# Optimization experiments

Measured on AMD Instinct MI355X. Metric: run time of the kernel, lower is better.

## Reference

```python
import jax, jax.numpy as jnp
import numpy as np

B, IC, H, W = 1024, 3, 32, 32
E, NC = 8, 100            # num_experts, num_classes
GCH, ECH = 16, 32         # gate hidden channels, expert hidden channels
K = 3                     # conv kernel size


def _conv2d(x, w):
    # x: [B,Cin,H,W], w: [Cout,Cin,kh,kw] -> [B,Cout,H,W] (SAME padding, stride 1)
    return jax.lax.conv_general_dilated(
        x, w, window_strides=(1, 1), padding='SAME',
        dimension_numbers=('NCHW', 'OIHW', 'NCHW'))


def setup_inputs() -> dict:
    key = jax.random.key(0)
    ks = jax.random.split(key, 9)
    init = lambda k, shape, fan: (jax.random.normal(k, shape, jnp.float32)
                                  * np.float32(1.0 / np.sqrt(fan)))
    return {
        'x': jax.random.normal(ks[0], (B, IC, H, W), jnp.float32),
        # GatingNetwork: conv(3->16) + relu + global-avg-pool + linear(16->E) + softmax
        'gate_conv_w': init(ks[1], (GCH, IC, K, K), IC * K * K),
        'gate_conv_b': jnp.zeros((GCH,), jnp.float32),
        'gate_lin_w': init(ks[2], (E, GCH), GCH),
        'gate_lin_b': jnp.zeros((E,), jnp.float32),
        # ExpertLayer (per expert): conv(3->32) + relu + global-avg-pool + linear(32->NC)
        'exp_conv_w': init(ks[3], (E, ECH, IC, K, K), IC * K * K),
        'exp_conv_b': jnp.zeros((E, ECH), jnp.float32),
        'exp_lin_w': init(ks[4], (E, NC, ECH), ECH),
        'exp_lin_b': jnp.zeros((E, NC), jnp.float32),
    }


def reference(x, gate_conv_w, gate_conv_b, gate_lin_w, gate_lin_b,
              exp_conv_w, exp_conv_b, exp_lin_w, exp_lin_b):
    # ---- Router: softmax gate over experts ----
    g = jax.nn.relu(_conv2d(x, gate_conv_w) + gate_conv_b[None, :, None, None])
    g = g.mean(axis=(2, 3))                                   # [B,GCH]
    weights = jax.nn.softmax(g @ gate_lin_w.T + gate_lin_b, axis=1)  # [B,E]
    best = jnp.argmax(weights, axis=1)                        # [B] hard top-1

    # ---- All experts as one fused conv (dense compute, then hard select) ----
    e, ch, ic, kh, kw = exp_conv_w.shape
    w_all = exp_conv_w.reshape(e * ch, ic, kh, kw)
    feat = _conv2d(x, w_all)                                  # [B,E*ECH,H,W]
    feat = feat.reshape(x.shape[0], e, ch, feat.shape[2], feat.shape[3])
    feat = jax.nn.relu(feat + exp_conv_b[None, :, :, None, None])
    pooled = feat.mean(axis=(3, 4))                           # [B,E,ECH]
    out_all = jnp.einsum('bec,enc->ben', pooled, exp_lin_w) + exp_lin_b[None]  # [B,E,NC]

    # Combine: each row gets only its argmax expert's output (others -> zero grad)
    final = jnp.take_along_axis(out_all, best[:, None, None], axis=1)[:, 0, :]  # [B,NC]
    return (final, weights)
```

## Files before the change

### kernel.cpp

```cpp
#include <hip/hip_runtime.h>
#include <math.h>

#define NB 1024
#define IC 3
#define HW 32
#define GCH 16
#define ECH 32
#define NE 8
#define NC 100

#define CS 38
#define RS2 114
#define NTX 3876

typedef __attribute__((ext_vector_type(8))) short bf16x8;
typedef __attribute__((ext_vector_type(4))) int   int4v;
typedef __attribute__((ext_vector_type(4))) float f32x4;

__device__ inline short f2bf(float f) {
    unsigned u = __float_as_uint(f);
    unsigned r = (u + 0x7FFF + ((u >> 16) & 1)) >> 16;
    return (short)r;
}
__device__ inline float bf2f(short h) {
    return __uint_as_float(((unsigned)(unsigned short)h) << 16);
}

__global__ __launch_bounds__(256) void moe_fused_kernel(
    const float* __restrict__ x,
    const float* __restrict__ gcw,
    const float* __restrict__ gcb,
    const float* __restrict__ glw,
    const float* __restrict__ glb,
    const float* __restrict__ ecw,
    const float* __restrict__ ecb,
    const float* __restrict__ elw,
    const float* __restrict__ elb,
    float* __restrict__ out_final,
    float* __restrict__ out_w)
{
    __shared__ __align__(16) int xil[NTX];
    __shared__ float red2[4][32];
    __shared__ float pg[GCH];
    __shared__ float pe[ECH];
    __shared__ int s_best;

    const int t = threadIdx.x;
    const int b = blockIdx.x;
    const int lane = t & 63;
    const int wid = t >> 6;
    const int r15 = lane & 15;
    const int kg = lane >> 4;
    const bool k3 = (kg == 3);
    const int kgoff = k3 ? 0 : kg * CS;

    for (int i = t; i < NTX / 4; i += 256) ((int4*)xil)[i] = make_int4(0, 0, 0, 0);

    bf16x8 gbh, gbl;
    #pragma unroll
    for (int r = 0; r < 8; ++r) {
        float w = 0.f;
        if (kg < 3) w = gcw[r15 * 27 + kg * 9 + r];
        else if (r < 3) w = gcw[r15 * 27 + r * 9 + 8];
        short h = f2bf(w);
        gbh[r] = h;
        gbl[r] = f2bf(w - bf2f(h));
    }
    const float gb = gcb[r15];

    __syncthreads();

    const float* xb = x + (size_t)b * (IC * HW * HW);
    #pragma unroll
    for (int i3 = 0; i3 < 3; ++i3) {
        int i = t + i3 * 256;
        float4 v = ((const float4*)xb)[i];
        int ci = i >> 8, rem = i & 255, row = rem >> 3, x4 = (rem & 7) << 2;
        int T = (row + 1) * RS2 + ci * CS + x4 + 2;
        short h0 = f2bf(v.x), h1 = f2bf(v.y), h2 = f2bf(v.z), h3 = f2bf(v.w);
        int t0 = (unsigned short)h0 | ((unsigned)(unsigned short)f2bf(v.x - bf2f(h0)) << 16);
        int t1 = (unsigned short)h1 | ((unsigned)(unsigned short)f2bf(v.y - bf2f(h1)) << 16);
        int t2 = (unsigned short)h2 | ((unsigned)(unsigned short)f2bf(v.z - bf2f(h2)) << 16);
        int t3 = (unsigned short)h3 | ((unsigned)(unsigned short)f2bf(v.w - bf2f(h3)) << 16);
        *(int2*)&xil[T]     = make_int2(t0, t1);
        *(int2*)&xil[T + 2] = make_int2(t2, t3);
    }

    __syncthreads();

    float sg = 0.f;
    #pragma unroll 2
    for (int m = 0; m < 16; ++m) {
        int px = (wid << 8) + (m << 4) + r15;
        int rowbase = (px >> 5) * RS2 + (px & 31) + 1;
        int vA = rowbase + kgoff;
        int vB = rowbase + 2 * RS2;
        int T0 = xil[vA];           int T1 = xil[vA + 1];
        int T2 = xil[vA + 2];       int T3 = xil[vA + RS2];
        int T4 = xil[vA + RS2 + 1]; int T5 = xil[vA + RS2 + 2];
        int T6 = xil[vA + 2 * RS2]; int T7 = xil[vA + 2 * RS2 + 1];
        int U0 = xil[vB + 2];       int U1 = xil[vB + 2 + CS];
        int U2 = xil[vB + 2 + 2 * CS];
        int X0 = k3 ? U0 : T0;
        int X1 = k3 ? U1 : T1;
        int X2 = k3 ? U2 : T2;
        int4v ahd = { (int)__builtin_amdgcn_perm(X1, X0, 0x05040100u),
                      (int)__builtin_amdgcn_perm(T3, X2, 0x05040100u),
                      (int)__builtin_amdgcn_perm(T5, T4, 0x05040100u),
                      (int)__builtin_amdgcn_perm(T7, T6, 0x05040100u) };
        int4v ald = { (int)__builtin_amdgcn_perm(X1, X0, 0x07060302u),
                      (int)__builtin_amdgcn_perm(T3, X2, 0x07060302u),
                      (int)__builtin_amdgcn_perm(T5, T4, 0x07060302u),
                      (int)__builtin_amdgcn_perm(T7, T6, 0x07060302u) };
        bf16x8 ah = __builtin_bit_cast(bf16x8, ahd);
        bf16x8 al = __builtin_bit_cast(bf16x8, ald);
        f32x4 d = {0.f, 0.f, 0.f, 0.f};
        d = __builtin_amdgcn_mfma_f32_16x16x32_bf16(al, gbh, d, 0, 0, 0);
        d = __builtin_amdgcn_mfma_f32_16x16x32_bf16(ah, gbl, d, 0, 0, 0);
        d = __builtin_amdgcn_mfma_f32_16x16x32_bf16(ah, gbh, d, 0, 0, 0);
        sg += fmaxf(d[0] + gb, 0.f) + fmaxf(d[1] + gb, 0.f) +
              fmaxf(d[2] + gb, 0.f) + fmaxf(d[3] + gb, 0.f);
    }
    {
        float v = sg;
        v += __shfl_xor(v, 16);
        v += __shfl_xor(v, 32);
        if (lane < 16) red2[wid][lane] = v;
    }
    __syncthreads();
    if (t < GCH)
        pg[t] = (red2[0][t] + red2[1][t] + red2[2][t] + red2[3][t]) * (1.f / 1024.f);
    __syncthreads();

    if (t < NE) {
        float acc = glb[t];
        #pragma unroll
        for (int c = 0; c < GCH; ++c) acc += pg[c] * glw[t * GCH + c];
        float m = acc;
        #pragma unroll
        for (int o = 1; o < NE; o <<= 1) m = fmaxf(m, __shfl_xor(m, o));
        float ex = expf(acc - m);
        float s = ex;
        #pragma unroll
        for (int o = 1; o < NE; o <<= 1) s += __shfl_xor(s, o);
        out_w[(size_t)b * NE + t] = ex / s;
        float mv = acc; int mi = t;
        #pragma unroll
        for (int o = 1; o < NE; o <<= 1) {
            float ov = __shfl_xor(mv, o);
            int   oi = __shfl_xor(mi, o);
            if (ov > mv || (ov == mv && oi < mi)) { mv = ov; mi = oi; }
        }
        if (t == 0) s_best = mi;
    }
    __syncthreads();
    const int e = __builtin_amdgcn_readfirstlane(s_best);

    const float* ewp = ecw + (size_t)e * (ECH * 27);
    const float* ebp = ecb + (size_t)e * ECH;

    bf16x8 bfr0, bfr1;
    #pragma unroll
    for (int r = 0; r < 8; ++r) {
        float w0 = 0.f, w1 = 0.f;
        if (kg < 3) {
            w0 = ewp[r15 * 27 + kg * 9 + r];
            w1 = ewp[(16 + r15) * 27 + kg * 9 + r];
        } else if (r < 3) {
            w0 = ewp[r15 * 27 + r * 9 + 8];
            w1 = ewp[(16 + r15) * 27 + r * 9 + 8];
        }
        bfr0[r] = f2bf(w0);
        bfr1[r] = f2bf(w1);
    }
    const float b0 = ebp[r15];
    const float b1 = ebp[16 + r15];

    float s0 = 0.f, s1 = 0.f;
    #pragma unroll 2
    for (int m = 0; m < 16; ++m) {
        int px = (wid << 8) + (m << 4) + r15;
        int rowbase = (px >> 5) * RS2 + (px & 31) + 1;
        int vA = rowbase + kgoff;
        int vB = rowbase + 2 * RS2;
        int T0 = xil[vA];           int T1 = xil[vA + 1];
        int T2 = xil[vA + 2];       int T3 = xil[vA + RS2];
        int T4 = xil[vA + RS2 + 1]; int T5 = xil[vA + RS2 + 2];
        int T6 = xil[vA + 2 * RS2]; int T7 = xil[vA + 2 * RS2 + 1];
        int U0 = xil[vB + 2];       int U1 = xil[vB + 2 + CS];
        int U2 = xil[vB + 2 + 2 * CS];
        int X0 = k3 ? U0 : T0;
        int X1 = k3 ? U1 : T1;
        int X2 = k3 ? U2 : T2;
        int4v ahd = { (int)__builtin_amdgcn_perm(X1, X0, 0x05040100u),
                      (int)__builtin_amdgcn_perm(T3, X2, 0x05040100u),
                      (int)__builtin_amdgcn_perm(T5, T4, 0x05040100u),
                      (int)__builtin_amdgcn_perm(T7, T6, 0x05040100u) };
        bf16x8 a = __builtin_bit_cast(bf16x8, ahd);
        f32x4 z = {0.f, 0.f, 0.f, 0.f};
        f32x4 d0 = __builtin_amdgcn_mfma_f32_16x16x32_bf16(a, bfr0, z, 0, 0, 0);
        f32x4 d1 = __builtin_amdgcn_mfma_f32_16x16x32_bf16(a, bfr1, z, 0, 0, 0);
        s0 += fmaxf(d0[0] + b0, 0.f) + fmaxf(d0[1] + b0, 0.f) +
              fmaxf(d0[2] + b0, 0.f) + fmaxf(d0[3] + b0, 0.f);
        s1 += fmaxf(d1[0] + b1, 0.f) + fmaxf(d1[1] + b1, 0.f) +
              fmaxf(d1[2] + b1, 0.f) + fmaxf(d1[3] + b1, 0.f);
    }
    {
        float v0 = s0, v1 = s1;
        v0 += __shfl_xor(v0, 16); v0 += __shfl_xor(v0, 32);
        v1 += __shfl_xor(v1, 16); v1 += __shfl_xor(v1, 32);
        if (lane < 16) { red2[wid][lane] = v0; red2[wid][lane + 16] = v1; }
    }
    __syncthreads();
    if (t < ECH)
        pe[t] = (red2[0][t] + red2[1][t] + red2[2][t] + red2[3][t]) * (1.f / 1024.f);
    __syncthreads();

    if (t < NC) {
        const float* lw = elw + ((size_t)e * NC + t) * ECH;
        float acc = elb[e * NC + t];
        #pragma unroll
        for (int c = 0; c < ECH; ++c) acc += pe[c] * lw[c];
        out_final[(size_t)b * NC + t] = acc;
    }
}

extern "C" void kernel_launch(void* const* d_in, const int* in_sizes, int n_in,
                              void* d_out, int out_size, void* d_ws, size_t ws_size,
                              hipStream_t stream) {
    const float* x   = (const float*)d_in[0];
    const float* gcw = (const float*)d_in[1];
    const float* gcb = (const float*)d_in[2];
    const float* glw = (const float*)d_in[3];
    const float* glb = (const float*)d_in[4];
    const float* ecw = (const float*)d_in[5];
    const float* ecb = (const float*)d_in[6];
    const float* elw = (const float*)d_in[7];
    const float* elb = (const float*)d_in[8];

    float* out_final = (float*)d_out;
    float* out_w     = (float*)d_out + NB * NC;

    hipLaunchKernelGGL(moe_fused_kernel, dim3(NB), dim3(256), 0, stream,
                       x, gcw, gcb, glw, glb, ecw, ecb, elw, elb,
                       out_final, out_w);
}
```

Before: 19.83 us.

## Process two samples per block to amortize setup and interleave MFMA chains

Each 256-thread block now handles two batch samples instead of one, which halves the grid to 512 blocks and doubles the LDS tile. Gate and expert convolutions for both samples are interleaved in the same loop, so independent MFMA chains can overlap, and the weight-fragment setup and barriers are shared across two samples. The cost is more registers and LDS per block and only 512 blocks, which may leave some of the 256 CUs with fewer waves to hide latency.

New measurement: 23.37 us. 17.9% more time.

```diff
diff --git a/kernel.cpp b/kernel.cpp
--- a/kernel.cpp
+++ b/kernel.cpp
@@ -39,14 +39,15 @@
     float* __restrict__ out_final,
     float* __restrict__ out_w)
 {
-    __shared__ __align__(16) int xil[NTX];
-    __shared__ float red2[4][32];
-    __shared__ float pg[GCH];
-    __shared__ float pe[ECH];
-    __shared__ int s_best;
+    __shared__ __align__(16) int xil[2 * NTX];
+    __shared__ float red2[4][64];
+    __shared__ float pg[2][GCH];
+    __shared__ float pe[2][ECH];
+    __shared__ int s_best[2];
 
     const int t = threadIdx.x;
-    const int b = blockIdx.x;
+    const int bA = 2 * blockIdx.x;
+    const int bB = bA + 1;
     const int lane = t & 63;
     const int wid = t >> 6;
     const int r15 = lane & 15;
@@ -54,7 +55,8 @@
     const bool k3 = (kg == 3);
     const int kgoff = k3 ? 0 : kg * CS;
 
-    for (int i = t; i < NTX / 4; i += 256) ((int4*)xil)[i] = make_int4(0, 0, 0, 0);
+    for (int i = t; i < (2 * NTX) / 4; i += 256)
+        ((int4*)xil)[i] = make_int4(0, 0, 0, 0);
 
     bf16x8 gbh, gbl;
     #pragma unroll
@@ -70,13 +72,16 @@
 
     __syncthreads();
 
-    const float* xb = x + (size_t)b * (IC * HW * HW);
+    const float* xbA = x + (size_t)bA * (IC * HW * HW);
+    const float* xbB = x + (size_t)bB * (IC * HW * HW);
     #pragma unroll
-    for (int i3 = 0; i3 < 3; ++i3) {
-        int i = t + i3 * 256;
-        float4 v = ((const float4*)xb)[i];
-        int ci = i >> 8, rem = i & 255, row = rem >> 3, x4 = (rem & 7) << 2;
-        int T = (row + 1) * RS2 + ci * CS + x4 + 2;
+    for (int i6 = 0; i6 < 6; ++i6) {
+        int i = t + i6 * 256;
+        int smp = (i >= 768);
+        int ii = i - (smp ? 768 : 0);
+        float4 v = smp ? ((const float4*)xbB)[ii] : ((const float4*)xbA)[ii];
+        int ci = ii >> 8, rem = ii & 255, row = rem >> 3, x4 = (rem & 7) << 2;
+        int T = (smp ? NTX : 0) + (row + 1) * RS2 + ci * CS + x4 + 2;
         short h0 = f2bf(v.x), h1 = f2bf(v.y), h2 = f2bf(v.z), h3 = f2bf(v.w);
         int t0 = (unsigned short)h0 | ((unsigned)(unsigned short)f2bf(v.x - bf2f(h0)) << 16);
         int t1 = (unsigned short)h1 | ((unsigned)(unsigned short)f2bf(v.y - bf2f(h1)) << 16);
@@ -88,140 +93,209 @@
 
     __syncthreads();
 
-    float sg = 0.f;
-    #pragma unroll 2
+    float sgA = 0.f, sgB = 0.f;
+    #pragma unroll 1
     for (int m = 0; m < 16; ++m) {
         int px = (wid << 8) + (m << 4) + r15;
         int rowbase = (px >> 5) * RS2 + (px & 31) + 1;
         int vA = rowbase + kgoff;
         int vB = rowbase + 2 * RS2;
-        int T0 = xil[vA];           int T1 = xil[vA + 1];
-        int T2 = xil[vA + 2];       int T3 = xil[vA + RS2];
-        int T4 = xil[vA + RS2 + 1]; int T5 = xil[vA + RS2 + 2];
-        int T6 = xil[vA + 2 * RS2]; int T7 = xil[vA + 2 * RS2 + 1];
-        int U0 = xil[vB + 2];       int U1 = xil[vB + 2 + CS];
-        int U2 = xil[vB + 2 + 2 * CS];
-        int X0 = k3 ? U0 : T0;
-        int X1 = k3 ? U1 : T1;
-        int X2 = k3 ? U2 : T2;
-        int4v ahd = { (int)__builtin_amdgcn_perm(X1, X0, 0x05040100u),
-                      (int)__builtin_amdgcn_perm(T3, X2, 0x05040100u),
-                      (int)__builtin_amdgcn_perm(T5, T4, 0x05040100u),
-                      (int)__builtin_amdgcn_perm(T7, T6, 0x05040100u) };
-        int4v ald = { (int)__builtin_amdgcn_perm(X1, X0, 0x07060302u),
-                      (int)__builtin_amdgcn_perm(T3, X2, 0x07060302u),
-                      (int)__builtin_amdgcn_perm(T5, T4, 0x07060302u),
-                      (int)__builtin_amdgcn_perm(T7, T6, 0x07060302u) };
-        bf16x8 ah = __builtin_bit_cast(bf16x8, ahd);
-        bf16x8 al = __builtin_bit_cast(bf16x8, ald);
-        f32x4 d = {0.f, 0.f, 0.f, 0.f};
-        d = __builtin_amdgcn_mfma_f32_16x16x32_bf16(al, gbh, d, 0, 0, 0);
-        d = __builtin_amdgcn_mfma_f32_16x16x32_bf16(ah, gbl, d, 0, 0, 0);
-        d = __builtin_amdgcn_mfma_f32_16x16x32_bf16(ah, gbh, d, 0, 0, 0);
-        sg += fmaxf(d[0] + gb, 0.f) + fmaxf(d[1] + gb, 0.f) +
-              fmaxf(d[2] + gb, 0.f) + fmaxf(d[3] + gb, 0.f);
+
+        int TA0 = xil[vA];           int TA1 = xil[vA + 1];
+        int TA2 = xil[vA + 2];       int TA3 = xil[vA + RS2];
+        int TA4 = xil[vA + RS2 + 1]; int TA5 = xil[vA + RS2 + 2];
+        int TA6 = xil[vA + 2 * RS2]; int TA7 = xil[vA + 2 * RS2 + 1];
+        int UA0 = xil[vB + 2];       int UA1 = xil[vB + 2 + CS];
+        int UA2 = xil[vB + 2 + 2 * CS];
+        int wA = vA + NTX, wB = vB + NTX;
+        int TB0 = xil[wA];           int TB1 = xil[wA + 1];
+        int TB2 = xil[wA + 2];       int TB3 = xil[wA + RS2];
+        int TB4 = xil[wA + RS2 + 1]; int TB5 = xil[wA + RS2 + 2];
+        int TB6 = xil[wA + 2 * RS2]; int TB7 = xil[wA + 2 * RS2 + 1];
+        int UB0 = xil[wB + 2];       int UB1 = xil[wB + 2 + CS];
+        int UB2 = xil[wB + 2 + 2 * CS];
+
+        int XA0 = k3 ? UA0 : TA0;  int XA1 = k3 ? UA1 : TA1;  int XA2 = k3 ? UA2 : TA2;
+        int XB0 = k3 ? UB0 : TB0;  int XB1 = k3 ? UB1 : TB1;  int XB2 = k3 ? UB2 : TB2;
+
+        int4v ahdA = { (int)__builtin_amdgcn_perm(XA1, XA0, 0x05040100u),
+                       (int)__builtin_amdgcn_perm(TA3, XA2, 0x05040100u),
+                       (int)__builtin_amdgcn_perm(TA5, TA4, 0x05040100u),
+                       (int)__builtin_amdgcn_perm(TA7, TA6, 0x05040100u) };
+        int4v aldA = { (int)__builtin_amdgcn_perm(XA1, XA0, 0x07060302u),
+                       (int)__builtin_amdgcn_perm(TA3, XA2, 0x07060302u),
+                       (int)__builtin_amdgcn_perm(TA5, TA4, 0x07060302u),
+                       (int)__builtin_amdgcn_perm(TA7, TA6, 0x07060302u) };
+        int4v ahdB = { (int)__builtin_amdgcn_perm(XB1, XB0, 0x05040100u),
+                       (int)__builtin_amdgcn_perm(TB3, XB2, 0x05040100u),
+                       (int)__builtin_amdgcn_perm(TB5, TB4, 0x05040100u),
+                       (int)__builtin_amdgcn_perm(TB7, TB6, 0x05040100u) };
+        int4v aldB = { (int)__builtin_amdgcn_perm(XB1, XB0, 0x07060302u),
+                       (int)__builtin_amdgcn_perm(TB3, XB2, 0x07060302u),
+                       (int)__builtin_amdgcn_perm(TB5, TB4, 0x07060302u),
+                       (int)__builtin_amdgcn_perm(TB7, TB6, 0x07060302u) };
+        bf16x8 ahA = __builtin_bit_cast(bf16x8, ahdA);
+        bf16x8 alA = __builtin_bit_cast(bf16x8, aldA);
+        bf16x8 ahB = __builtin_bit_cast(bf16x8, ahdB);
+        bf16x8 alB = __builtin_bit_cast(bf16x8, aldB);
+
+        f32x4 dA = {0.f, 0.f, 0.f, 0.f};
+        f32x4 dB = {0.f, 0.f, 0.f, 0.f};
+        dA = __builtin_amdgcn_mfma_f32_16x16x32_bf16(alA, gbh, dA, 0, 0, 0);
+        dB = __builtin_amdgcn_mfma_f32_16x16x32_bf16(alB, gbh, dB, 0, 0, 0);
+        dA = __builtin_amdgcn_mfma_f32_16x16x32_bf16(ahA, gbl, dA, 0, 0, 0);
+        dB = __builtin_amdgcn_mfma_f32_16x16x32_bf16(ahB, gbl, dB, 0, 0, 0);
+        dA = __builtin_amdgcn_mfma_f32_16x16x32_bf16(ahA, gbh, dA, 0, 0, 0);
+        dB = __builtin_amdgcn_mfma_f32_16x16x32_bf16(ahB, gbh, dB, 0, 0, 0);
+        sgA += fmaxf(dA[0] + gb, 0.f) + fmaxf(dA[1] + gb, 0.f) +
+               fmaxf(dA[2] + gb, 0.f) + fmaxf(dA[3] + gb, 0.f);
+        sgB += fmaxf(dB[0] + gb, 0.f) + fmaxf(dB[1] + gb, 0.f) +
+               fmaxf(dB[2] + gb, 0.f) + fmaxf(dB[3] + gb, 0.f);
     }
     {
-        float v = sg;
-        v += __shfl_xor(v, 16);
-        v += __shfl_xor(v, 32);
-        if (lane < 16) red2[wid][lane] = v;
-    }
-    __syncthreads();
-    if (t < GCH)
-        pg[t] = (red2[0][t] + red2[1][t] + red2[2][t] + red2[3][t]) * (1.f / 1024.f);
-    __syncthreads();
-
-    if (t < NE) {
-        float acc = glb[t];
-        #pragma unroll
-        for (int c = 0; c < GCH; ++c) acc += pg[c] * glw[t * GCH + c];
+        float vA2 = sgA, vB2 = sgB;
+        vA2 += __shfl_xor(vA2, 16); vA2 += __shfl_xor(vA2, 32);
+        vB2 += __shfl_xor(vB2, 16); vB2 += __shfl_xor(vB2, 32);
+        if (lane < 16) { red2[wid][lane] = vA2; red2[wid][lane + 32] = vB2; }
+    }
+    __syncthreads();
+    if (t < 32) {
+        int s = t >> 4, c = t & 15;
+        int col = s * 32 + c;
+        pg[s][c] = (red2[0][col] + red2[1][col] + red2[2][col] + red2[3][col])
+                   * (1.f / 1024.f);
+    }
+    __syncthreads();
+
+    if (t < 16) {
+        int s = t >> 3, ee = t & 7;
+        float acc = glb[ee];
+        #pragma unroll
+        for (int c = 0; c < GCH; ++c) acc += pg[s][c] * glw[ee * GCH + c];
         float m = acc;
         #pragma unroll
         for (int o = 1; o < NE; o <<= 1) m = fmaxf(m, __shfl_xor(m, o));
         float ex = expf(acc - m);
-        float s = ex;
-        #pragma unroll
-        for (int o = 1; o < NE; o <<= 1) s += __shfl_xor(s, o);
-        out_w[(size_t)b * NE + t] = ex / s;
-        float mv = acc; int mi = t;
+        float ssum = ex;
+        #pragma unroll
+        for (int o = 1; o < NE; o <<= 1) ssum += __shfl_xor(ssum, o);
+        out_w[(size_t)(s ? bB : bA) * NE + ee] = ex / ssum;
+        float mv = acc; int mi = ee;
         #pragma unroll
         for (int o = 1; o < NE; o <<= 1) {
             float ov = __shfl_xor(mv, o);
             int   oi = __shfl_xor(mi, o);
             if (ov > mv || (ov == mv && oi < mi)) { mv = ov; mi = oi; }
         }
-        if (t == 0) s_best = mi;
-    }
-    __syncthreads();
-    const int e = __builtin_amdgcn_readfirstlane(s_best);
-
-    const float* ewp = ecw + (size_t)e * (ECH * 27);
-    const float* ebp = ecb + (size_t)e * ECH;
-
-    bf16x8 bfr0, bfr1;
+        if (ee == 0) s_best[s] = mi;
+    }
+    __syncthreads();
+    const int eA = __builtin_amdgcn_readfirstlane(s_best[0]);
+    const int eB = __builtin_amdgcn_readfirstlane(s_best[1]);
+
+    const float* ewpA = ecw + (size_t)eA * (ECH * 27);
+    const float* ewpB = ecw + (size_t)eB * (ECH * 27);
+    const float* ebpA = ecb + (size_t)eA * ECH;
+    const float* ebpB = ecb + (size_t)eB * ECH;
+
+    bf16x8 bA0, bA1, bB0, bB1;
     #pragma unroll
     for (int r = 0; r < 8; ++r) {
-        float w0 = 0.f, w1 = 0.f;
+        float wa0 = 0.f, wa1 = 0.f, wb0 = 0.f, wb1 = 0.f;
         if (kg < 3) {
-            w0 = ewp[r15 * 27 + kg * 9 + r];
-            w1 = ewp[(16 + r15) * 27 + kg * 9 + r];
+            wa0 = ewpA[r15 * 27 + kg * 9 + r];
+            wa1 = ewpA[(16 + r15) * 27 + kg * 9 + r];
+            wb0 = ewpB[r15 * 27 + kg * 9 + r];
+            wb1 = ewpB[(16 + r15) * 27 + kg * 9 + r];
         } else if (r < 3) {
-            w0 = ewp[r15 * 27 + r * 9 + 8];
-            w1 = ewp[(16 + r15) * 27 + r * 9 + 8];
+            wa0 = ewpA[r15 * 27 + r * 9 + 8];
+            wa1 = ewpA[(16 + r15) * 27 + r * 9 + 8];
+            wb0 = ewpB[r15 * 27 + r * 9 + 8];
+            wb1 = ewpB[(16 + r15) * 27 + r * 9 + 8];
         }
-        bfr0[r] = f2bf(w0);
-        bfr1[r] = f2bf(w1);
-    }
-    const float b0 = ebp[r15];
-    const float b1 = ebp[16 + r15];
-
-    float s0 = 0.f, s1 = 0.f;
-    #pragma unroll 2
+        bA0[r] = f2bf(wa0); bA1[r] = f2bf(wa1);
+        bB0[r] = f2bf(wb0); bB1[r] = f2bf(wb1);
+    }
+    const float c0A = ebpA[r15], c1A = ebpA[16 + r15];
+    const float c0B = ebpB[r15], c1B = ebpB[16 + r15];
+
+    float s0A = 0.f, s1A = 0.f, s0B = 0.f, s1B = 0.f;
+    #pragma unroll 1
     for (int m = 0; m < 16; ++m) {
         int px = (wid << 8) + (m << 4) + r15;
         int rowbase = (px >> 5) * RS2 + (px & 31) + 1;
         int vA = rowbase + kgoff;
         int vB = rowbase + 2 * RS2;
-        int T0 = xil[vA];           int T1 = xil[vA + 1];
-        int T2 = xil[vA + 2];       int T3 = xil[vA + RS2];
-        int T4 = xil[vA + RS2 + 1]; int T5 = xil[vA + RS2 + 2];
-        int T6 = xil[vA + 2 * RS2]; int T7 = xil[vA + 2 * RS2 + 1];
-        int U0 = xil[vB + 2];       int U1 = xil[vB + 2 + CS];
-        int U2 = xil[vB + 2 + 2 * CS];
-        int X0 = k3 ? U0 : T0;
-        int X1 = k3 ? U1 : T1;
-        int X2 = k3 ? U2 : T2;
-        int4v ahd = { (int)__builtin_amdgcn_perm(X1, X0, 0x05040100u),
-                      (int)__builtin_amdgcn_perm(T3, X2, 0x05040100u),
-                      (int)__builtin_amdgcn_perm(T5, T4, 0x05040100u),
-                      (int)__builtin_amdgcn_perm(T7, T6, 0x05040100u) };
-        bf16x8 a = __builtin_bit_cast(bf16x8, ahd);
+        int TA0 = xil[vA];           int TA1 = xil[vA + 1];
+        int TA2 = xil[vA + 2];       int TA3 = xil[vA + RS2];
+        int TA4 = xil[vA + RS2 + 1]; int TA5 = xil[vA + RS2 + 2];
+        int TA6 = xil[vA + 2 * RS2]; int TA7 = xil[vA + 2 * RS2 + 1];
+        int UA0 = xil[vB + 2];       int UA1 = xil[vB + 2 + CS];
+        int UA2 = xil[vB + 2 + 2 * CS];
+        int wA = vA + NTX, wB = vB + NTX;
+        int TB0 = xil[wA];           int TB1 = xil[wA + 1];
+        int TB2 = xil[wA + 2];       int TB3 = xil[wA + RS2];
+        int TB4 = xil[wA + RS2 + 1]; int TB5 = xil[wA + RS2 + 2];
+        int TB6 = xil[wA + 2 * RS2]; int TB7 = xil[wA + 2 * RS2 + 1];
+        int UB0 = xil[wB + 2];       int UB1 = xil[wB + 2 + CS];
+        int UB2 = xil[wB + 2 + 2 * CS];
+
+        int XA0 = k3 ? UA0 : TA0;  int XA1 = k3 ? UA1 : TA1;  int XA2 = k3 ? UA2 : TA2;
+        int XB0 = k3 ? UB0 : TB0;  int XB1 = k3 ? UB1 : TB1;  int XB2 = k3 ? UB2 : TB2;
+
+        int4v ahdA = { (int)__builtin_amdgcn_perm(XA1, XA0, 0x05040100u),
+                       (int)__builtin_amdgcn_perm(TA3, XA2, 0x05040100u),
+                       (int)__builtin_amdgcn_perm(TA5, TA4, 0x05040100u),
+                       (int)__builtin_amdgcn_perm(TA7, TA6, 0x05040100u) };
+        int4v ahdB = { (int)__builtin_amdgcn_perm(XB1, XB0, 0x05040100u),
+                       (int)__builtin_amdgcn_perm(TB3, XB2, 0x05040100u),
+                       (int)__builtin_amdgcn_perm(TB5, TB4, 0x05040100u),
+                       (int)__builtin_amdgcn_perm(TB7, TB6, 0x05040100u) };
+        bf16x8 aA = __builtin_bit_cast(bf16x8, ahdA);
+        bf16x8 aB = __builtin_bit_cast(bf16x8, ahdB);
         f32x4 z = {0.f, 0.f, 0.f, 0.f};
-        f32x4 d0 = __builtin_amdgcn_mfma_f32_16x16x32_bf16(a, bfr0, z, 0, 0, 0);
-        f32x4 d1 = __builtin_amdgcn_mfma_f32_16x16x32_bf16(a, bfr1, z, 0, 0, 0);
-        s0 += fmaxf(d0[0] + b0, 0.f) + fmaxf(d0[1] + b0, 0.f) +
-              fmaxf(d0[2] + b0, 0.f) + fmaxf(d0[3] + b0, 0.f);
-        s1 += fmaxf(d1[0] + b1, 0.f) + fmaxf(d1[1] + b1, 0.f) +
-              fmaxf(d1[2] + b1, 0.f) + fmaxf(d1[3] + b1, 0.f);
+        f32x4 d0A = __builtin_amdgcn_mfma_f32_16x16x32_bf16(aA, bA0, z, 0, 0, 0);
+        f32x4 d0B = __builtin_amdgcn_mfma_f32_16x16x32_bf16(aB, bB0, z, 0, 0, 0);
+        f32x4 d1A = __builtin_amdgcn_mfma_f32_16x16x32_bf16(aA, bA1, z, 0, 0, 0);
+        f32x4 d1B = __builtin_amdgcn_mfma_f32_16x16x32_bf16(aB, bB1, z, 0, 0, 0);
+        s0A += fmaxf(d0A[0] + c0A, 0.f) + fmaxf(d0A[1] + c0A, 0.f) +
+               fmaxf(d0A[2] + c0A, 0.f) + fmaxf(d0A[3] + c0A, 0.f);
+        s1A += fmaxf(d1A[0] + c1A, 0.f) + fmaxf(d1A[1] + c1A, 0.f) +
+               fmaxf(d1A[2] + c1A, 0.f) + fmaxf(d1A[3] + c1A, 0.f);
+        s0B += fmaxf(d0B[0] + c0B, 0.f) + fmaxf(d0B[1] + c0B, 0.f) +
+               fmaxf(d0B[2] + c0B, 0.f) + fmaxf(d0B[3] + c0B, 0.f);
+        s1B += fmaxf(d1B[0] + c1B, 0.f) + fmaxf(d1B[1] + c1B, 0.f) +
+               fmaxf(d1B[2] + c1B, 0.f) + fmaxf(d1B[3] + c1B, 0.f);
     }
     {
-        float v0 = s0, v1 = s1;
-        v0 += __shfl_xor(v0, 16); v0 += __shfl_xor(v0, 32);
-        v1 += __shfl_xor(v1, 16); v1 += __shfl_xor(v1, 32);
-        if (lane < 16) { red2[wid][lane] = v0; red2[wid][lane + 16] = v1; }
-    }
-    __syncthreads();
-    if (t < ECH)
-        pe[t] = (red2[0][t] + red2[1][t] + red2[2][t] + red2[3][t]) * (1.f / 1024.f);
-    __syncthreads();
-
-    if (t < NC) {
-        const float* lw = elw + ((size_t)e * NC + t) * ECH;
-        float acc = elb[e * NC + t];
-        #pragma unroll
-        for (int c = 0; c < ECH; ++c) acc += pe[c] * lw[c];
-        out_final[(size_t)b * NC + t] = acc;
+        float v0A = s0A, v1A = s1A, v0B = s0B, v1B = s1B;
+        v0A += __shfl_xor(v0A, 16); v0A += __shfl_xor(v0A, 32);
+        v1A += __shfl_xor(v1A, 16); v1A += __shfl_xor(v1A, 32);
+        v0B += __shfl_xor(v0B, 16); v0B += __shfl_xor(v0B, 32);
+        v1B += __shfl_xor(v1B, 16); v1B += __shfl_xor(v1B, 32);
+        if (lane < 16) {
+            red2[wid][lane]      = v0A;
+            red2[wid][lane + 16] = v1A;
+            red2[wid][lane + 32] = v0B;
+            red2[wid][lane + 48] = v1B;
+        }
+    }
+    __syncthreads();
+    if (t < 64) {
+        pe[t >> 5][t & 31] = (red2[0][t] + red2[1][t] + red2[2][t] + red2[3][t])
+                             * (1.f / 1024.f);
+    }
+    __syncthreads();
+
+    if (t < 200) {
+        int s = (t >= 100) ? 1 : 0;
+        int c = t - s * 100;
+        int es = s ? eB : eA;
+        const float* lw = elw + ((size_t)es * NC + c) * ECH;
+        float acc = elb[es * NC + c];
+        #pragma unroll
+        for (int ch = 0; ch < ECH; ++ch) acc += pe[s][ch] * lw[ch];
+        out_final[(size_t)(s ? bB : bA) * NC + c] = acc;
     }
 }
 
@@ -241,7 +315,7 @@
     float* out_final = (float*)d_out;
     float* out_w     = (float*)d_out + NB * NC;
 
-    hipLaunchKernelGGL(moe_fused_kernel, dim3(NB), dim3(256), 0, stream,
+    hipLaunchKernelGGL(moe_fused_kernel, dim3(NB / 2), dim3(256), 0, stream,
                        x, gcw, gcb, glw, glb, ecw, ecb, elw, elb,
                        out_final, out_w);
 }
```
